# Performance work log

Measured on AMD Instinct MI355X. Metric: run time of the kernel, lower is better.

The kernel has to match this reference:

```python
import jax, jax.numpy as jnp
import numpy as np

N, E, G = 50000, 800000, 64
IN, H, ED, OUT = 32, 96, 16, 128
EPS_GEN = 1e-7   # GENConv message eps
EPS_BN = 1e-5    # BatchNorm1d eps


def _bn(x, g, b):
    # training-mode BatchNorm1d: batch stats, biased variance
    mu = jnp.mean(x, axis=0)
    var = jnp.var(x, axis=0)
    return (x - mu) * jax.lax.rsqrt(var + EPS_BN) * g + b


def _genconv(x_src, x_dst, src, dst, ea, mw1, mg, mb, mw2):
    # message: relu(x_j + e_ij) + eps            [E, H]
    msg = jax.nn.relu(x_src[src] + ea) + EPS_GEN
    n = x_dst.shape[0]
    # softmax aggregation over incoming edges per dst node (t=1.0)
    m = jax.ops.segment_max(msg, dst, num_segments=n)
    ex = jnp.exp(msg - m[dst])
    s = jax.ops.segment_sum(ex, dst, num_segments=n)
    agg = jax.ops.segment_sum(msg * (ex / s[dst]), dst, num_segments=n)
    h = agg + x_dst
    # GENConv internal MLP: Lin(H,2H,no bias) -> BN -> ReLU -> Lin(2H,H,no bias)
    h = jax.nn.relu(_bn(h @ mw1, mg, mb))
    return h @ mw2


def _forward(x, edge_attr, w_src1, w_dst1, w_edge1,
             mlp1_w1, mlp1_g, mlp1_b, mlp1_w2, bn1_g, bn1_b,
             w_edge2, mlp2_w1, mlp2_g, mlp2_b, mlp2_w2, bn2_g, bn2_b,
             w_edge3, mlp3_w1, mlp3_g, mlp3_b, mlp3_w2, bn3_g, bn3_b,
             lin_w, lin_b, edge_index, batch):
    src, dst = edge_index[0], edge_index[1]
    h = _genconv(x @ w_src1, x @ w_dst1, src, dst, edge_attr @ w_edge1,
                 mlp1_w1, mlp1_g, mlp1_b, mlp1_w2)
    h = jax.nn.relu(_bn(h, bn1_g, bn1_b))
    h = _genconv(h, h, src, dst, edge_attr @ w_edge2,
                 mlp2_w1, mlp2_g, mlp2_b, mlp2_w2)
    h = jax.nn.relu(_bn(h, bn2_g, bn2_b))
    h = _genconv(h, h, src, dst, edge_attr @ w_edge3,
                 mlp3_w1, mlp3_g, mlp3_b, mlp3_w2)
    h = jax.nn.relu(_bn(h, bn3_g, bn3_b))
    # global mean pool over graphs (dropout is identity in eval)
    cnt = jax.ops.segment_sum(jnp.ones((h.shape[0],), h.dtype), batch, num_segments=G)
    pooled = jax.ops.segment_sum(h, batch, num_segments=G) / jnp.maximum(cnt, 1.0)[:, None]
    return pooled @ lin_w + lin_b


def setup_inputs() -> dict:
    key = jax.random.key(0)
    ks = jax.random.split(key, 20)
    rn = lambda i, shp, s=0.05: jax.random.normal(ks[i], shp, jnp.float32) * s
    return {
        'x': rn(0, (N, IN), 1.0),
        'edge_attr': rn(1, (E, ED), 1.0),
        'edge_index': jax.random.randint(ks[2], (2, E), 0, N, jnp.int32),
        'batch': jnp.sort(jax.random.randint(ks[3], (N,), 0, G, jnp.int32)),
        'w_src1': rn(4, (IN, H)), 'w_dst1': rn(5, (IN, H)), 'w_edge1': rn(6, (ED, H)),
        'mlp1_w1': rn(7, (H, 2 * H)), 'mlp1_g': jnp.ones(2 * H), 'mlp1_b': jnp.zeros(2 * H),
        'mlp1_w2': rn(8, (2 * H, H)), 'bn1_g': jnp.ones(H), 'bn1_b': jnp.zeros(H),
        'w_edge2': rn(9, (ED, H)),
        'mlp2_w1': rn(10, (H, 2 * H)), 'mlp2_g': jnp.ones(2 * H), 'mlp2_b': jnp.zeros(2 * H),
        'mlp2_w2': rn(11, (2 * H, H)), 'bn2_g': jnp.ones(H), 'bn2_b': jnp.zeros(H),
        'w_edge3': rn(12, (ED, H)),
        'mlp3_w1': rn(13, (H, 2 * H)), 'mlp3_g': jnp.ones(2 * H), 'mlp3_b': jnp.zeros(2 * H),
        'mlp3_w2': rn(14, (2 * H, H)), 'bn3_g': jnp.ones(H), 'bn3_b': jnp.zeros(H),
        'lin_w': rn(15, (H, OUT)), 'lin_b': jnp.zeros(OUT),
    }


def reference(x, edge_attr, edge_index, batch, w_src1, w_dst1, w_edge1,
              mlp1_w1, mlp1_g, mlp1_b, mlp1_w2, bn1_g, bn1_b,
              w_edge2, mlp2_w1, mlp2_g, mlp2_b, mlp2_w2, bn2_g, bn2_b,
              w_edge3, mlp3_w1, mlp3_g, mlp3_b, mlp3_w2, bn3_g, bn3_b,
              lin_w, lin_b):
    return _forward(x, edge_attr, w_src1, w_dst1, w_edge1,
                    mlp1_w1, mlp1_g, mlp1_b, mlp1_w2, bn1_g, bn1_b,
                    w_edge2, mlp2_w1, mlp2_g, mlp2_b, mlp2_w2, bn2_g, bn2_b,
                    w_edge3, mlp3_w1, mlp3_g, mlp3_b, mlp3_w2, bn3_g, bn3_b,
                    lin_w, lin_b, edge_index, batch)
```

## Files before the change

### kernel.cpp

```cpp
#include <hip/hip_runtime.h>
#include <math.h>

#define NN 50000
#define EE 800000
#define GG 64
#define HH 96
#define H2 192
#define INF 32
#define EDF 16
#define OUTF 128
#define EPS_GEN 1e-7f
#define EPS_BN 1e-5f
#define NPB 100
#define NB_SCAN 49
#define NBH (256 * NB_SCAN)
#define BSCAN_PT 13
#define LOG2E 1.44269504088896f
#define SHIFT2 28.85390081777927f
#define GRIDP 512
#define NT64 ((NN + 63) / 64)
#define PROJ_GRID 1024

typedef _Float16 f16;
typedef _Float16 f16x2 __attribute__((ext_vector_type(2)));
typedef _Float16 f16x8 __attribute__((ext_vector_type(8)));
typedef float f32x4 __attribute__((ext_vector_type(4)));

static inline size_t align256(size_t x) { return (x + 255) & ~(size_t)255; }

__device__ __forceinline__ float fdot2(f16x2 a, f16x2 b, float c) {
#if __has_builtin(__builtin_amdgcn_fdot2)
    return __builtin_amdgcn_fdot2(a, b, c, false);
#else
    return fmaf((float)a.x, (float)b.x, fmaf((float)a.y, (float)b.y, c));
#endif
}

__device__ __forceinline__ float exp2fast(float x) {
#if __has_builtin(__builtin_amdgcn_exp2f)
    return __builtin_amdgcn_exp2f(x);
#else
    return exp2f(x);
#endif
}

union W8 { float4 f[2]; f16x2 h[8]; };
union EAu { float4 f; f16x2 h[4]; };
union XUu { float2 f; f16x2 h[2]; };

__device__ __forceinline__ void agg_step(const EAu& e0, const EAu& e1, const XUu& xu,
                                         const W8* w, float* num, float* den) {
    float xv[4] = {(float)xu.h[0].x, (float)xu.h[0].y, (float)xu.h[1].x, (float)xu.h[1].y};
    #pragma unroll
    for (int cc = 0; cc < 4; ++cc) {
        float acc = 0.f;
        #pragma unroll
        for (int k = 0; k < 4; ++k) acc = fdot2(e0.h[k], w[cc].h[k], acc);
        #pragma unroll
        for (int k = 0; k < 4; ++k) acc = fdot2(e1.h[k], w[cc].h[4 + k], acc);
        float msg = fmaxf(xv[cc] + acc, 0.f) + EPS_GEN;
        float p = exp2fast(fmaf(msg, LOG2E, -SHIFT2));
        den[cc] += p;
        num[cc] = fmaf(msg, p, num[cc]);
    }
}


__global__ __launch_bounds__(256) void hist_kernel(const int* __restrict__ dst,
                                                   int* __restrict__ deg,
                                                   int* __restrict__ rank) {
    int e = blockIdx.x * 256 + threadIdx.x;
    if (e >= EE) return;
    rank[e] = atomicAdd(&deg[dst[e]], 1);
}

__global__ __launch_bounds__(1024) void scan1_kernel(const int* __restrict__ deg,
                                                     int* __restrict__ offs,
                                                     int* __restrict__ bsum,
                                                     int* __restrict__ bhist) {
    __shared__ int ws[16];
    __shared__ int lh[256];
    int tid = threadIdx.x, lane = tid & 63, w = tid >> 6;
    if (tid < 256) lh[tid] = 0;
    int i = blockIdx.x * 1024 + tid;
    int v = (i < NN) ? deg[i] : 0;
    __syncthreads();
    if (i < NN) {
        int b = 255 - (v > 255 ? 255 : v);
        atomicAdd(&lh[b], 1);
    }
    int x = v;
    #pragma unroll
    for (int off = 1; off < 64; off <<= 1) {
        int y = __shfl_up(x, off, 64);
        if (lane >= off) x += y;
    }
    if (lane == 63) ws[w] = x;
    __syncthreads();
    int wpre = 0;
    for (int j = 0; j < w; ++j) wpre += ws[j];
    if (i < NN) offs[i] = wpre + x - v;
    if (tid == 1023) bsum[blockIdx.x] = wpre + x;
    if (tid < 256) bhist[tid * NB_SCAN + blockIdx.x] = lh[tid];
}

__global__ __launch_bounds__(1024) void bscan_kernel(int* __restrict__ bhist,
                                                     int* __restrict__ bsum,
                                                     float* __restrict__ pool) {
    __shared__ int ws[16];
    int tid = threadIdx.x, lane = tid & 63, w = tid >> 6;
    for (int i = tid; i < GG * HH; i += 1024) pool[i] = 0.f;
    if (tid < 64) {
        int v = (tid < NB_SCAN) ? bsum[tid] : 0;
        int x = v;
        #pragma unroll
        for (int off = 1; off < 64; off <<= 1) {
            int y = __shfl_up(x, off, 64);
            if (lane >= off) x += y;
        }
        if (tid < NB_SCAN) bsum[tid] = x - v;
    }
    int base = tid * BSCAN_PT;
    int loc[BSCAN_PT];
    int s = 0;
    #pragma unroll
    for (int i = 0; i < BSCAN_PT; ++i) {
        int idx = base + i;
        int v = (idx < NBH) ? bhist[idx] : 0;
        loc[i] = s;
        s += v;
    }
    int x = s;
    #pragma unroll
    for (int off = 1; off < 64; off <<= 1) {
        int y = __shfl_up(x, off, 64);
        if (lane >= off) x += y;
    }
    if (lane == 63) ws[w] = x;
    __syncthreads();
    int wpre = 0;
    for (int j = 0; j < w; ++j) wpre += ws[j];
    int pre = wpre + x - s;
    #pragma unroll
    for (int i = 0; i < BSCAN_PT; ++i) {
        int idx = base + i;
        if (idx < NBH) bhist[idx] = pre + loc[i];
    }
}

__global__ __launch_bounds__(1024) void finsort_kernel(int* __restrict__ offs,
                                                       const int* __restrict__ bsum,
                                                       const int* __restrict__ deg,
                                                       const int* __restrict__ bhist,
                                                       int* __restrict__ perm) {
    __shared__ int cnt[256];
    int tid = threadIdx.x;
    if (tid < 256) cnt[tid] = 0;
    __syncthreads();
    int n = blockIdx.x * 1024 + tid;
    if (n < NN) {
        offs[n] += bsum[blockIdx.x];
        int d = deg[n];
        int b = 255 - (d > 255 ? 255 : d);
        int rank = atomicAdd(&cnt[b], 1);
        perm[bhist[b * NB_SCAN + blockIdx.x] + rank] = n;
    }
    if (n == NN) offs[NN] = EE;
}

__global__ __launch_bounds__(256) void scatter_kernel(const int* __restrict__ src,
                                                      const int* __restrict__ dst,
                                                      const int* __restrict__ offs,
                                                      const int* __restrict__ rank,
                                                      const float* __restrict__ eattr,
                                                      int* __restrict__ csr_src,
                                                      float4* __restrict__ csrea) {
    int e = blockIdx.x * 256 + threadIdx.x;
    if (e >= EE) return;
    int d = dst[e];
    int slot = offs[d] + rank[e];
    csr_src[slot] = src[e];
    const float4* ep = (const float4*)(eattr + (size_t)e * EDF);
    float4 v0 = ep[0], v1 = ep[1], v2 = ep[2], v3 = ep[3];
    union { f16x2 h[4]; float4 f; } a, b;
    a.h[0] = f16x2{(f16)v0.x, (f16)v0.y};
    a.h[1] = f16x2{(f16)v0.z, (f16)v0.w};
    a.h[2] = f16x2{(f16)v1.x, (f16)v1.y};
    a.h[3] = f16x2{(f16)v1.z, (f16)v1.w};
    b.h[0] = f16x2{(f16)v2.x, (f16)v2.y};
    b.h[1] = f16x2{(f16)v2.z, (f16)v2.w};
    b.h[2] = f16x2{(f16)v3.x, (f16)v3.y};
    b.h[3] = f16x2{(f16)v3.z, (f16)v3.w};
    csrea[(size_t)slot * 2] = a.f;
    csrea[(size_t)slot * 2 + 1] = b.f;
}

__global__ __launch_bounds__(256) void wprep_kernel(
    const float* __restrict__ we0, const float* __restrict__ we1, const float* __restrict__ we2,
    const float* __restrict__ m10, const float* __restrict__ m11, const float* __restrict__ m12,
    const float* __restrict__ m20, const float* __restrict__ m21, const float* __restrict__ m22,
    f16* __restrict__ wte, f16* __restrict__ wt1, f16* __restrict__ wt2,
    int* __restrict__ csr_src) {
    int idx = blockIdx.x * 256 + threadIdx.x;
    if (idx < 8) csr_src[EE + idx] = 0;
    if (idx < 4608) {
        const float* w = (idx < 1536) ? we0 : ((idx < 3072) ? we1 : we2);
        int r = idx % 1536, c = r / EDF, k = r % EDF;
        wte[idx] = (f16)w[k * HH + c];
    } else if (idx < 4608 + 3 * 18432) {
        int m = idx - 4608;
        const float* w = (m < 18432) ? m10 : ((m < 36864) ? m11 : m12);
        int r = m % 18432, j = r / HH, k = r % HH;
        wt1[m] = (f16)w[k * H2 + j];
    } else if (idx < 4608 + 6 * 18432) {
        int m = idx - 4608 - 3 * 18432;
        const float* w = (m < 18432) ? m20 : ((m < 36864) ? m21 : m22);
        int r = m % 18432, j = r / H2, k = r % H2;
        wt2[m] = (f16)w[k * HH + j];
    }
}


__global__ __launch_bounds__(256) void proj_kernel(const float* __restrict__ x,
                                                   const float* __restrict__ ws,
                                                   const float* __restrict__ wd,
                                                   f16* __restrict__ xs,
                                                   f16* __restrict__ xd) {
    __shared__ float Ws[INF * HH], Wd[INF * HH];
    int tid = threadIdx.x;
    for (int i = tid; i < INF * HH; i += 256) { Ws[i] = ws[i]; Wd[i] = wd[i]; }
    __syncthreads();
    for (int gid = blockIdx.x * 256 + tid; gid < NN * HH; gid += PROJ_GRID * 256) {
        int n = gid / HH, c = gid % HH;
        const float* xr = x + (size_t)n * INF;
        float as = 0.f, ad = 0.f;
        #pragma unroll
        for (int k = 0; k < INF; ++k) {
            float xv = xr[k];
            as = fmaf(xv, Ws[k * HH + c], as);
            ad = fmaf(xv, Wd[k * HH + c], ad);
        }
        xs[gid] = (f16)as;
        xd[gid] = (f16)ad;
    }
}


#define AGG_LOAD(E0, E1, XU, JJ, SR)                                    \
    E0.f = csrea[(size_t)(JJ) * 2];                                     \
    E1.f = csrea[(size_t)(JJ) * 2 + 1];                                 \
    XU.f = *(const float2*)(xsrc + (size_t)(SR) * HH + c0);

__global__ __launch_bounds__(192) void agg_kernel(const f16* __restrict__ xsrc,
                                                  const f16* __restrict__ xdst,
                                                  const float4* __restrict__ csrea,
                                                  const f16* __restrict__ wt,
                                                  const int* __restrict__ offs,
                                                  const int* __restrict__ csr_src,
                                                  const int* __restrict__ perm,
                                                  float* __restrict__ stats,
                                                  f16* __restrict__ hpre) {
    int tid = threadIdx.x;
    if (blockIdx.x == 0) {
        for (int t = tid; t < 576; t += 192) stats[t] = 0.f;
    }
    int idx = blockIdx.x * 8 + tid / 24;
    if (idx >= NN) return;
    int node = perm[idx];
    int cg = tid % 24, c0 = cg * 4;
    W8 w[4];
    #pragma unroll
    for (int cc = 0; cc < 4; ++cc) {
        const float4* wp = (const float4*)(wt + (c0 + cc) * EDF);
        w[cc].f[0] = wp[0];
        w[cc].f[1] = wp[1];
    }
    XUu xd;
    xd.f = *(const float2*)(xdst + (size_t)node * HH + c0);
    int s0 = offs[node], s1 = offs[node + 1];
    float num[4] = {0.f, 0.f, 0.f, 0.f}, den[4] = {0.f, 0.f, 0.f, 0.f};
    if (s0 < s1) {
        int last = s1 - 1;
        EAu eA0, eA1, eB0, eB1, eC0, eC1;
        XUu xA, xB, xC;
        int sA = csr_src[s0], sB = csr_src[s0 + 1], sC = csr_src[s0 + 2];
        AGG_LOAD(eA0, eA1, xA, s0, sA)
        AGG_LOAD(eB0, eB1, xB, s0 + 1, sB)
        AGG_LOAD(eC0, eC1, xC, s0 + 2, sC)
        int sD = csr_src[s0 + 3], sE = csr_src[s0 + 4], sF = csr_src[s0 + 5];
        for (int j = s0; j < s1; j += 3) {
            __builtin_amdgcn_s_setprio(1);
            agg_step(eA0, eA1, xA, w, num, den);
            __builtin_amdgcn_s_setprio(0);
            AGG_LOAD(eA0, eA1, xA, j + 3, sD)
            sD = csr_src[j + 6];
            if (j + 1 <= last) {
                __builtin_amdgcn_s_setprio(1);
                agg_step(eB0, eB1, xB, w, num, den);
                __builtin_amdgcn_s_setprio(0);
            }
            AGG_LOAD(eB0, eB1, xB, j + 4, sE)
            sE = csr_src[j + 7];
            if (j + 2 <= last) {
                __builtin_amdgcn_s_setprio(1);
                agg_step(eC0, eC1, xC, w, num, den);
                __builtin_amdgcn_s_setprio(0);
            }
            AGG_LOAD(eC0, eC1, xC, j + 5, sF)
            sF = csr_src[j + 8];
        }
    }
    float xdv[4] = {(float)xd.h[0].x, (float)xd.h[0].y, (float)xd.h[1].x, (float)xd.h[1].y};
    float r0 = (den[0] > 0.f) ? num[0] / den[0] : 0.f;
    float r1 = (den[1] > 0.f) ? num[1] / den[1] : 0.f;
    float r2 = (den[2] > 0.f) ? num[2] / den[2] : 0.f;
    float r3 = (den[3] > 0.f) ? num[3] / den[3] : 0.f;
    union { float2 f; f16x2 h[2]; } o;
    o.h[0] = f16x2{(f16)(r0 + xdv[0]), (f16)(r1 + xdv[1])};
    o.h[1] = f16x2{(f16)(r2 + xdv[2]), (f16)(r3 + xdv[3])};
    *(float2*)(hpre + (size_t)node * HH + c0) = o.f;
}

#define LDA1 104

__global__ __launch_bounds__(256) void gemm1_kernel(const f16* __restrict__ A,
                                                    const f16* __restrict__ Wt,
                                                    f16* __restrict__ T,
                                                    float* __restrict__ colsum,
                                                    float* __restrict__ colsumsq) {
    __shared__ f16 Al[64 * LDA1];
    __shared__ f16 Wl[192 * LDA1];
    __shared__ float red[H2 * 2];
    int tid = threadIdx.x;
    for (int v = tid; v < 192 * 12; v += 256) {
        int r = v / 12, c8 = (v % 12) * 8;
        *(float4*)(Wl + r * LDA1 + c8) = *(const float4*)(Wt + r * HH + c8);
    }
    for (int t = tid; t < H2 * 2; t += 256) red[t] = 0.f;
    __syncthreads();
    int wv = tid >> 6, l = tid & 63, lr = l & 15, lg = l >> 4;
    int i0 = wv * 16;
    for (int tile = blockIdx.x; tile < NT64; tile += GRIDP) {
        int n0 = tile * 64;
        for (int v = tid; v < 64 * 12; v += 256) {
            int r = v / 12, c8 = (v % 12) * 8;
            float4 d = {0.f, 0.f, 0.f, 0.f};
            if (n0 + r < NN) d = *(const float4*)(A + (size_t)(n0 + r) * HH + c8);
            *(float4*)(Al + r * LDA1 + c8) = d;
        }
        __syncthreads();
        f32x4 acc[12];
        #pragma unroll
        for (int t = 0; t < 12; ++t) acc[t] = (f32x4){0.f, 0.f, 0.f, 0.f};
        #pragma unroll
        for (int ks = 0; ks < 3; ++ks) {
            int k0 = ks * 32 + lg * 8;
            f16x8 af = *(const f16x8*)(Al + (i0 + lr) * LDA1 + k0);
            #pragma unroll
            for (int t = 0; t < 12; ++t) {
                f16x8 bf = *(const f16x8*)(Wl + (t * 16 + lr) * LDA1 + k0);
                acc[t] = __builtin_amdgcn_mfma_f32_16x16x32_f16(af, bf, acc[t], 0, 0, 0);
            }
        }
        #pragma unroll
        for (int t = 0; t < 12; ++t) {
            int col = t * 16 + lr;
            float s = 0.f, q = 0.f;
            #pragma unroll
            for (int rr = 0; rr < 4; ++rr) {
                int row = n0 + i0 + lg * 4 + rr;
                float v = acc[t][rr];
                if (row < NN) {
                    T[(size_t)row * H2 + col] = (f16)v;
                    s += v;
                    q = fmaf(v, v, q);
                }
            }
            s += __shfl_xor(s, 16); s += __shfl_xor(s, 32);
            q += __shfl_xor(q, 16); q += __shfl_xor(q, 32);
            if (lg == 0) { atomicAdd(&red[col], s); atomicAdd(&red[H2 + col], q); }
        }
        __syncthreads();
    }
    if (tid < H2) {
        atomicAdd(&colsum[tid], red[tid]);
        atomicAdd(&colsumsq[tid], red[H2 + tid]);
    }
}

#define LDA2 200

__global__ __launch_bounds__(256) void gemm2_kernel(const f16* __restrict__ T,
                                                    const f16* __restrict__ Wt,
                                                    const float* __restrict__ cs1,
                                                    const float* __restrict__ cq1,
                                                    const float* __restrict__ g1,
                                                    const float* __restrict__ b1,
                                                    f16* __restrict__ U,
                                                    float* __restrict__ colsum,
                                                    float* __restrict__ colsumsq) {
    __shared__ f16 Al[64 * LDA2];
    __shared__ f16 Wl[96 * LDA2];
    __shared__ float ab[H2 * 2];
    __shared__ float red[HH * 2];
    int tid = threadIdx.x;
    if (tid < H2) {
        const float invN = 1.f / (float)NN;
        float mu = cs1[tid] * invN;
        float var = fmaxf(cq1[tid] * invN - mu * mu, 0.f);
        float a = g1[tid] * rsqrtf(var + EPS_BN);
        ab[tid] = a;
        ab[H2 + tid] = b1[tid] - mu * a;
    }
    if (tid < HH * 2) red[tid] = 0.f;
    for (int v = tid; v < 96 * 24; v += 256) {
        int r = v / 24, c8 = (v % 24) * 8;
        *(float4*)(Wl + r * LDA2 + c8) = *(const float4*)(Wt + r * H2 + c8);
    }
    __syncthreads();
    int wv = tid >> 6, l = tid & 63, lr = l & 15, lg = l >> 4;
    int i0 = wv * 16;
    for (int tile = blockIdx.x; tile < NT64; tile += GRIDP) {
        int n0 = tile * 64;
        for (int v = tid; v < 64 * 24; v += 256) {
            int r = v / 24, c8 = (v % 24) * 8;
            float4 dd = {0.f, 0.f, 0.f, 0.f};
            if (n0 + r < NN) {
                union { float4 f; f16x2 h[4]; } u, o;
                u.f = *(const float4*)(T + (size_t)(n0 + r) * H2 + c8);
                #pragma unroll
                for (int p = 0; p < 4; ++p) {
                    float x0 = fmaxf(fmaf((float)u.h[p].x, ab[c8 + 2 * p], ab[H2 + c8 + 2 * p]), 0.f);
                    float x1 = fmaxf(fmaf((float)u.h[p].y, ab[c8 + 2 * p + 1], ab[H2 + c8 + 2 * p + 1]), 0.f);
                    o.h[p] = f16x2{(f16)x0, (f16)x1};
                }
                dd = o.f;
            }
            *(float4*)(Al + r * LDA2 + c8) = dd;
        }
        __syncthreads();
        f32x4 acc[6];
        #pragma unroll
        for (int t = 0; t < 6; ++t) acc[t] = (f32x4){0.f, 0.f, 0.f, 0.f};
        #pragma unroll
        for (int ks = 0; ks < 6; ++ks) {
            int k0 = ks * 32 + lg * 8;
            f16x8 af = *(const f16x8*)(Al + (i0 + lr) * LDA2 + k0);
            #pragma unroll
            for (int t = 0; t < 6; ++t) {
                f16x8 bf = *(const f16x8*)(Wl + (t * 16 + lr) * LDA2 + k0);
                acc[t] = __builtin_amdgcn_mfma_f32_16x16x32_f16(af, bf, acc[t], 0, 0, 0);
            }
        }
        #pragma unroll
        for (int t = 0; t < 6; ++t) {
            int col = t * 16 + lr;
            float s = 0.f, q = 0.f;
            #pragma unroll
            for (int rr = 0; rr < 4; ++rr) {
                int row = n0 + i0 + lg * 4 + rr;
                float v = acc[t][rr];
                if (row < NN) {
                    U[(size_t)row * HH + col] = (f16)v;
                    s += v;
                    q = fmaf(v, v, q);
                }
            }
            s += __shfl_xor(s, 16); s += __shfl_xor(s, 32);
            q += __shfl_xor(q, 16); q += __shfl_xor(q, 32);
            if (lg == 0) { atomicAdd(&red[col], s); atomicAdd(&red[HH + col], q); }
        }
        __syncthreads();
    }
    if (tid < HH) {
        atomicAdd(&colsum[tid], red[tid]);
        atomicAdd(&colsumsq[tid], red[HH + tid]);
    }
}


__global__ __launch_bounds__(256) void elem_kernel(const f16* __restrict__ U,
                                                   const float* __restrict__ cs2,
                                                   const float* __restrict__ cq2,
                                                   const float* __restrict__ g2,
                                                   const float* __restrict__ b2,
                                                   f16* __restrict__ Hout) {
    __shared__ float ab[HH * 2];
    int tid = threadIdx.x;
    if (tid < HH) {
        const float invN = 1.f / (float)NN;
        float mu = cs2[tid] * invN;
        float var = fmaxf(cq2[tid] * invN - mu * mu, 0.f);
        float a = g2[tid] * rsqrtf(var + EPS_BN);
        ab[tid] = a;
        ab[HH + tid] = b2[tid] - mu * a;
    }
    __syncthreads();
    int i = blockIdx.x * 256 + tid;
    if (i >= NN * HH / 8) return;
    union { float4 f; f16x2 h[4]; } u, o;
    u.f = ((const float4*)U)[i];
    int k = (i % 12) * 8;
    #pragma unroll
    for (int p = 0; p < 4; ++p) {
        float x0 = fmaxf(fmaf((float)u.h[p].x, ab[k + 2 * p], ab[HH + k + 2 * p]), 0.f);
        float x1 = fmaxf(fmaf((float)u.h[p].y, ab[k + 2 * p + 1], ab[HH + k + 2 * p + 1]), 0.f);
        o.h[p] = f16x2{(f16)x0, (f16)x1};
    }
    ((float4*)Hout)[i] = o.f;
}


__global__ __launch_bounds__(192) void pool_bn_kernel(const f16* __restrict__ U,
                                                      const float* __restrict__ cs2,
                                                      const float* __restrict__ cq2,
                                                      const float* __restrict__ g2,
                                                      const float* __restrict__ b2,
                                                      const int* __restrict__ batch,
                                                      float* __restrict__ pool) {
    __shared__ float ab[HH * 2];
    int tid = threadIdx.x;
    if (tid < HH) {
        const float invN = 1.f / (float)NN;
        float mu = cs2[tid] * invN;
        float var = fmaxf(cq2[tid] * invN - mu * mu, 0.f);
        float a = g2[tid] * rsqrtf(var + EPS_BN);
        ab[tid] = a;
        ab[HH + tid] = b2[tid] - mu * a;
    }
    __syncthreads();
    int n0 = blockIdx.x * NPB;
    int n1 = (n0 + NPB < NN) ? n0 + NPB : NN;
    int c = tid % HH;
    int h = tid / HH;
    float a_ = ab[c], b_ = ab[HH + c];
    float acc = 0.f;
    int gcur = -1;
    for (int n = n0 + h; n < n1; n += 2) {
        int g = batch[n];
        if (g != gcur) {
            if (gcur >= 0) atomicAdd(&pool[gcur * HH + c], acc);
            acc = 0.f;
            gcur = g;
        }
        acc += fmaxf(fmaf((float)U[(size_t)n * HH + c], a_, b_), 0.f);
    }
    if (gcur >= 0) atomicAdd(&pool[gcur * HH + c], acc);
}

__global__ __launch_bounds__(128) void out_kernel(const float* __restrict__ pool,
                                                  const int* __restrict__ batch,
                                                  const float* __restrict__ lw,
                                                  const float* __restrict__ lb,
                                                  float* __restrict__ out) {
    int g = blockIdx.x, o = threadIdx.x;
    int lo = 0, hi = NN;
    while (lo < hi) { int mid = (lo + hi) >> 1; if (batch[mid] < g) lo = mid + 1; else hi = mid; }
    int s = lo;
    lo = 0; hi = NN;
    while (lo < hi) { int mid = (lo + hi) >> 1; if (batch[mid] < g + 1) lo = mid + 1; else hi = mid; }
    float inv = 1.f / fmaxf((float)(lo - s), 1.f);
    float acc = lb[o];
    for (int c = 0; c < HH; ++c) acc = fmaf(pool[g * HH + c] * inv, lw[c * OUTF + o], acc);
    out[(size_t)g * OUTF + o] = acc;
}


extern "C" void kernel_launch(void* const* d_in, const int* in_sizes, int n_in,
                              void* d_out, int out_size, void* d_ws, size_t ws_size,
                              hipStream_t stream) {
    const float* x = (const float*)d_in[0];
    const float* eattr = (const float*)d_in[1];
    const int* eidx = (const int*)d_in[2];
    const int* batch = (const int*)d_in[3];
    const float* w_src1 = (const float*)d_in[4];
    const float* w_dst1 = (const float*)d_in[5];
    const float* w_e[3] = {(const float*)d_in[6], (const float*)d_in[13], (const float*)d_in[20]};
    const float* mw1[3] = {(const float*)d_in[7], (const float*)d_in[14], (const float*)d_in[21]};
    const float* mg[3] = {(const float*)d_in[8], (const float*)d_in[15], (const float*)d_in[22]};
    const float* mb[3] = {(const float*)d_in[9], (const float*)d_in[16], (const float*)d_in[23]};
    const float* mw2[3] = {(const float*)d_in[10], (const float*)d_in[17], (const float*)d_in[24]};
    const float* bng[3] = {(const float*)d_in[11], (const float*)d_in[18], (const float*)d_in[25]};
    const float* bnb[3] = {(const float*)d_in[12], (const float*)d_in[19], (const float*)d_in[26]};
    const float* lin_w = (const float*)d_in[27];
    const float* lin_b = (const float*)d_in[28];
    float* out = (float*)d_out;

    const int* src = eidx;
    const int* dst = eidx + EE;

    char* base = (char*)d_ws;
    size_t off = 0;
    int* deg = (int*)(base + off); off = align256(off + (size_t)NN * 4);
    int* rank = (int*)(base + off); off = align256(off + (size_t)EE * 4);
    int* offs = (int*)(base + off); off = align256(off + (size_t)(NN + 1) * 4);
    int* bsum = (int*)(base + off); off = align256(off + (size_t)NB_SCAN * 4);
    int* bhist = (int*)(base + off); off = align256(off + (size_t)NBH * 4);
    int* perm = (int*)(base + off); off = align256(off + (size_t)NN * 4);
    int* csr_src = (int*)(base + off); off = align256(off + (size_t)(EE + 8) * 4);
    float* stats = (float*)(base + off); off = align256(off + 576 * 4);
    float* colsum1 = stats;
    float* colsumsq1 = stats + 192;
    float* colsum2 = stats + 384;
    float* colsumsq2 = stats + 480;
    float* pool = (float*)(base + off); off = align256(off + (size_t)GG * HH * 4);
    f16* wte = (f16*)(base + off); off = align256(off + (size_t)3 * 1536 * 2);
    f16* wt1 = (f16*)(base + off); off = align256(off + (size_t)3 * 18432 * 2);
    f16* wt2 = (f16*)(base + off); off = align256(off + (size_t)3 * 18432 * 2);
    f16* XS = (f16*)(base + off); off = align256(off + (size_t)NN * HH * 2);
    f16* XD = (f16*)(base + off); off = align256(off + (size_t)NN * HH * 2);
    f16* HP = (f16*)(base + off); off = align256(off + (size_t)NN * HH * 2);
    f16* T = (f16*)(base + off); off = align256(off + (size_t)NN * H2 * 2);
    float4* csrea = (float4*)(base + off); off = align256(off + (size_t)(EE + 8) * 32);
    (void)in_sizes; (void)n_in; (void)out_size; (void)ws_size;

    hipMemsetAsync(deg, 0, (size_t)NN * 4, stream);
    hist_kernel<<<(EE + 255) / 256, 256, 0, stream>>>(dst, deg, rank);
    scan1_kernel<<<NB_SCAN, 1024, 0, stream>>>(deg, offs, bsum, bhist);
    bscan_kernel<<<1, 1024, 0, stream>>>(bhist, bsum, pool);
    finsort_kernel<<<NB_SCAN, 1024, 0, stream>>>(offs, bsum, deg, bhist, perm);
    scatter_kernel<<<(EE + 255) / 256, 256, 0, stream>>>(src, dst, offs, rank, eattr,
                                                         csr_src, csrea);
    wprep_kernel<<<(4608 + 6 * 18432 + 255) / 256, 256, 0, stream>>>(
        w_e[0], w_e[1], w_e[2], mw1[0], mw1[1], mw1[2], mw2[0], mw2[1], mw2[2],
        wte, wt1, wt2, csr_src);
    proj_kernel<<<PROJ_GRID, 256, 0, stream>>>(x, w_src1, w_dst1, XS, XD);

    for (int l = 0; l < 3; ++l) {
        const f16* xdst = (l == 0) ? XD : XS;
        agg_kernel<<<(NN + 7) / 8, 192, 0, stream>>>(XS, xdst, csrea, wte + l * 1536, offs,
                                                     csr_src, perm, stats, HP);
        gemm1_kernel<<<GRIDP, 256, 0, stream>>>(HP, wt1 + l * 18432, T, colsum1, colsumsq1);
        gemm2_kernel<<<GRIDP, 256, 0, stream>>>(T, wt2 + l * 18432, colsum1, colsumsq1,
                                                mg[l], mb[l], HP, colsum2, colsumsq2);
        if (l < 2)
            elem_kernel<<<(NN * HH / 8 + 255) / 256, 256, 0, stream>>>(HP, colsum2, colsumsq2,
                                                                       bng[l], bnb[l], XS);
    }

    pool_bn_kernel<<<(NN + NPB - 1) / NPB, 192, 0, stream>>>(HP, colsum2, colsumsq2,
                                                             bng[2], bnb[2], batch, pool);
    out_kernel<<<GG, 128, 0, stream>>>(pool, batch, lin_w, lin_b, out);
}
```

Before: 486.9 us.

## Widen aggregation to 8 channels per thread and precompute byte offsets

```diff
diff --git a/kernel.cpp b/kernel.cpp
--- a/kernel.cpp
+++ b/kernel.cpp
@@ -44,20 +44,22 @@
 #endif
 }
 
-union W8 { float4 f[2]; f16x2 h[8]; };
-union EAu { float4 f; f16x2 h[4]; };
-union XUu { float2 f; f16x2 h[2]; };
-
-__device__ __forceinline__ void agg_step(const EAu& e0, const EAu& e1, const XUu& xu,
-                                         const W8* w, float* num, float* den) {
-    float xv[4] = {(float)xu.h[0].x, (float)xu.h[0].y, (float)xu.h[1].x, (float)xu.h[1].y};
-    #pragma unroll
-    for (int cc = 0; cc < 4; ++cc) {
+union EA2 { float4 f[2]; f16x2 h[8]; };
+union XU2 { float4 f; f16x2 h[4]; };
+
+__device__ __forceinline__ void agg_step8(const EA2& e, const XU2& xu, const EA2* w,
+                                          float* num, float* den) {
+    float xv[8];
+    #pragma unroll
+    for (int p = 0; p < 4; ++p) {
+        xv[2 * p] = (float)xu.h[p].x;
+        xv[2 * p + 1] = (float)xu.h[p].y;
+    }
+    #pragma unroll
+    for (int cc = 0; cc < 8; ++cc) {
         float acc = 0.f;
         #pragma unroll
-        for (int k = 0; k < 4; ++k) acc = fdot2(e0.h[k], w[cc].h[k], acc);
-        #pragma unroll
-        for (int k = 0; k < 4; ++k) acc = fdot2(e1.h[k], w[cc].h[4 + k], acc);
+        for (int k = 0; k < 8; ++k) acc = fdot2(e.h[k], w[cc].h[k], acc);
         float msg = fmaxf(xv[cc] + acc, 0.f) + EPS_GEN;
         float p = exp2fast(fmaf(msg, LOG2E, -SHIFT2));
         den[cc] += p;
@@ -179,7 +181,7 @@
     if (e >= EE) return;
     int d = dst[e];
     int slot = offs[d] + rank[e];
-    csr_src[slot] = src[e];
+    csr_src[slot] = src[e] * (HH * 2);
     const float4* ep = (const float4*)(eattr + (size_t)e * EDF);
     float4 v0 = ep[0], v1 = ep[1], v2 = ep[2], v3 = ep[3];
     union { f16x2 h[4]; float4 f; } a, b;
@@ -246,10 +248,10 @@
 }
 
 
-#define AGG_LOAD(E0, E1, XU, JJ, SR)                                    \
-    E0.f = csrea[(size_t)(JJ) * 2];                                     \
-    E1.f = csrea[(size_t)(JJ) * 2 + 1];                                 \
-    XU.f = *(const float2*)(xsrc + (size_t)(SR) * HH + c0);
+#define AGG_LOAD8(E, XU, JJ, SO)                                         \
+    E.f[0] = csrea[(size_t)(JJ) * 2];                                    \
+    E.f[1] = csrea[(size_t)(JJ) * 2 + 1];                                \
+    XU.f = *(const float4*)(xsrcb + (size_t)(unsigned)(SO) + c0 * 2);
 
 __global__ __launch_bounds__(192) void agg_kernel(const f16* __restrict__ xsrc,
                                                   const f16* __restrict__ xdst,
@@ -264,61 +266,55 @@
     if (blockIdx.x == 0) {
         for (int t = tid; t < 576; t += 192) stats[t] = 0.f;
     }
-    int idx = blockIdx.x * 8 + tid / 24;
+    int idx = blockIdx.x * 16 + tid / 12;
     if (idx >= NN) return;
     int node = perm[idx];
-    int cg = tid % 24, c0 = cg * 4;
-    W8 w[4];
-    #pragma unroll
-    for (int cc = 0; cc < 4; ++cc) {
+    int cg = tid % 12, c0 = cg * 8;
+    const char* xsrcb = (const char*)xsrc;
+    EA2 w[8];
+    #pragma unroll
+    for (int cc = 0; cc < 8; ++cc) {
         const float4* wp = (const float4*)(wt + (c0 + cc) * EDF);
         w[cc].f[0] = wp[0];
         w[cc].f[1] = wp[1];
     }
-    XUu xd;
-    xd.f = *(const float2*)(xdst + (size_t)node * HH + c0);
+    XU2 xd;
+    xd.f = *(const float4*)(xdst + (size_t)node * HH + c0);
     int s0 = offs[node], s1 = offs[node + 1];
-    float num[4] = {0.f, 0.f, 0.f, 0.f}, den[4] = {0.f, 0.f, 0.f, 0.f};
+    float num[8] = {0.f, 0.f, 0.f, 0.f, 0.f, 0.f, 0.f, 0.f};
+    float den[8] = {0.f, 0.f, 0.f, 0.f, 0.f, 0.f, 0.f, 0.f};
     if (s0 < s1) {
         int last = s1 - 1;
-        EAu eA0, eA1, eB0, eB1, eC0, eC1;
-        XUu xA, xB, xC;
-        int sA = csr_src[s0], sB = csr_src[s0 + 1], sC = csr_src[s0 + 2];
-        AGG_LOAD(eA0, eA1, xA, s0, sA)
-        AGG_LOAD(eB0, eB1, xB, s0 + 1, sB)
-        AGG_LOAD(eC0, eC1, xC, s0 + 2, sC)
-        int sD = csr_src[s0 + 3], sE = csr_src[s0 + 4], sF = csr_src[s0 + 5];
-        for (int j = s0; j < s1; j += 3) {
+        EA2 eA, eB;
+        XU2 xA, xB;
+        int soA = csr_src[s0], soB = csr_src[s0 + 1];
+        AGG_LOAD8(eA, xA, s0, soA)
+        AGG_LOAD8(eB, xB, s0 + 1, soB)
+        int soC = csr_src[s0 + 2], soD = csr_src[s0 + 3];
+        for (int j = s0; j < s1; j += 2) {
             __builtin_amdgcn_s_setprio(1);
-            agg_step(eA0, eA1, xA, w, num, den);
+            agg_step8(eA, xA, w, num, den);
             __builtin_amdgcn_s_setprio(0);
-            AGG_LOAD(eA0, eA1, xA, j + 3, sD)
-            sD = csr_src[j + 6];
+            AGG_LOAD8(eA, xA, j + 2, soC)
+            soC = csr_src[j + 4];
             if (j + 1 <= last) {
                 __builtin_amdgcn_s_setprio(1);
-                agg_step(eB0, eB1, xB, w, num, den);
+                agg_step8(eB, xB, w, num, den);
                 __builtin_amdgcn_s_setprio(0);
             }
-            AGG_LOAD(eB0, eB1, xB, j + 4, sE)
-            sE = csr_src[j + 7];
-            if (j + 2 <= last) {
-                __builtin_amdgcn_s_setprio(1);
-                agg_step(eC0, eC1, xC, w, num, den);
-                __builtin_amdgcn_s_setprio(0);
-            }
-            AGG_LOAD(eC0, eC1, xC, j + 5, sF)
-            sF = csr_src[j + 8];
-        }
-    }
-    float xdv[4] = {(float)xd.h[0].x, (float)xd.h[0].y, (float)xd.h[1].x, (float)xd.h[1].y};
-    float r0 = (den[0] > 0.f) ? num[0] / den[0] : 0.f;
-    float r1 = (den[1] > 0.f) ? num[1] / den[1] : 0.f;
-    float r2 = (den[2] > 0.f) ? num[2] / den[2] : 0.f;
-    float r3 = (den[3] > 0.f) ? num[3] / den[3] : 0.f;
-    union { float2 f; f16x2 h[2]; } o;
-    o.h[0] = f16x2{(f16)(r0 + xdv[0]), (f16)(r1 + xdv[1])};
-    o.h[1] = f16x2{(f16)(r2 + xdv[2]), (f16)(r3 + xdv[3])};
-    *(float2*)(hpre + (size_t)node * HH + c0) = o.f;
+            AGG_LOAD8(eB, xB, j + 3, soD)
+            soD = csr_src[j + 5];
+        }
+    }
+    union { float4 f; f16x2 h[4]; } o;
+    #pragma unroll
+    for (int p = 0; p < 4; ++p) {
+        float xd0 = (float)xd.h[p].x, xd1 = (float)xd.h[p].y;
+        float r0 = (den[2 * p] > 0.f) ? num[2 * p] / den[2 * p] : 0.f;
+        float r1 = (den[2 * p + 1] > 0.f) ? num[2 * p + 1] / den[2 * p + 1] : 0.f;
+        o.h[p] = f16x2{(f16)(r0 + xd0), (f16)(r1 + xd1)};
+    }
+    *(float4*)(hpre + (size_t)node * HH + c0) = o.f;
 }
 
 #define LDA1 104
@@ -628,8 +624,8 @@
 
     for (int l = 0; l < 3; ++l) {
         const f16* xdst = (l == 0) ? XD : XS;
-        agg_kernel<<<(NN + 7) / 8, 192, 0, stream>>>(XS, xdst, csrea, wte + l * 1536, offs,
-                                                     csr_src, perm, stats, HP);
+        agg_kernel<<<(NN + 15) / 16, 192, 0, stream>>>(XS, xdst, csrea, wte + l * 1536, offs,
+                                                       csr_src, perm, stats, HP);
         gemm1_kernel<<<GRIDP, 256, 0, stream>>>(HP, wt1 + l * 18432, T, colsum1, colsumsq1);
         gemm2_kernel<<<GRIDP, 256, 0, stream>>>(T, wt2 + l * 18432, colsum1, colsumsq1,
                                                 mg[l], mb[l], HP, colsum2, colsumsq2);
```

New measurement: 498.4 us. 2.4% more time.
